# Optimization experiments

Measured on AMD Instinct MI355X. Metric: run time of the kernel, lower is better.

The kernel has to match this reference:

```python
import jax, jax.numpy as jnp
import numpy as np

N, E, IN_DIM, HID, OUT = 50000, 600000, 128, 256, 128

def setup_inputs() -> dict:
    key = jax.random.key(0)
    k1, k2, k3, k4, k5, k6, k7 = jax.random.split(key, 7)
    h = jax.random.normal(k1, (N, IN_DIM), dtype=jnp.float32)
    src = jax.random.randint(k2, (E,), 0, N)
    dst = jax.random.randint(k3, (E,), 0, N)
    s1 = 1.0 / np.sqrt(2 * IN_DIM)
    s2 = 1.0 / np.sqrt(HID)
    W1 = jax.random.uniform(k4, (2 * IN_DIM, HID), minval=-s1, maxval=s1, dtype=jnp.float32)
    b1 = jax.random.uniform(k5, (HID,), minval=-s1, maxval=s1, dtype=jnp.float32)
    W2 = jax.random.uniform(k6, (HID, OUT), minval=-s2, maxval=s2, dtype=jnp.float32)
    b2 = jax.random.uniform(k7, (OUT,), minval=-s2, maxval=s2, dtype=jnp.float32)
    return {"h": h, "src": src, "dst": dst, "W1": W1, "b1": b1, "W2": W2, "b2": b2}

def reference(h, src, dst, W1, b1, W2, b2):
    n = h.shape[0]
    # copy_u + mean: gather src features, segment-sum at dst, divide by in-degree
    msg_sum = jax.ops.segment_sum(h[src], dst, num_segments=n)          # [N, D]
    deg = jax.ops.segment_sum(jnp.ones((src.shape[0],), h.dtype), dst, num_segments=n)
    h_neigh = msg_sum / jnp.maximum(deg, 1.0)[:, None]                  # zero-deg nodes -> 0
    h_total = jnp.concatenate([h, h_neigh], axis=1)                     # [N, 2D]
    out = (h_total @ W1 + b1) @ W2 + b2                                 # 2-layer MLP (no inner activation)
    return jax.nn.relu(out)
```

## Files before the change

### kernel.cpp

```cpp
#include <hip/hip_runtime.h>

#define N_NODES 50000
#define E_EDGES 600000
#define IN_DIM  128
#define HID     256
#define OUT_DIM 128
#define CAP     64

#define NB_FILL 2344
#define NB_HCVT 6250
#define NB_WCVT 384

typedef __bf16 bf16x8 __attribute__((ext_vector_type(8)));
typedef float  f32x16 __attribute__((ext_vector_type(16)));

__device__ __forceinline__ unsigned short f2bf(float f) {
    union { float f; unsigned int i; } v; v.f = f;
    unsigned int b = v.i;
    b += 0x7fffu + ((b >> 16) & 1u);
    return (unsigned short)(b >> 16);
}
__device__ __forceinline__ float bf2f(unsigned short u) {
    union { unsigned int i; float f; } v; v.i = ((unsigned int)u) << 16; return v.f;
}

__global__ void __launch_bounds__(256)
sage_prep(const int* __restrict__ src, const int* __restrict__ dst,
          int* __restrict__ counts, int* __restrict__ bucket,
          const float* __restrict__ h, unsigned short* __restrict__ ht,
          const float* __restrict__ W1, const float* __restrict__ W2,
          unsigned short* __restrict__ w1sw, unsigned short* __restrict__ w2sw) {
    int b = blockIdx.x;
    if (b < NB_FILL) {
        int e = b * 256 + threadIdx.x;
        if (e < E_EDGES) {
            int d = dst[e];
            int slot = atomicAdd(counts + d, 1);
            if (slot < CAP) bucket[(size_t)d * CAP + slot] = src[e];
        }
    } else if (b < NB_FILL + NB_HCVT) {
        int idx = (b - NB_FILL) * 256 + threadIdx.x;
        if (idx < N_NODES * 32) {
            int n = idx >> 5, g = idx & 31;
            const float4 v = *(const float4*)(h + (size_t)n * IN_DIM + g * 4);
            ushort4 o;
            o.x = f2bf(v.x); o.y = f2bf(v.y); o.z = f2bf(v.z); o.w = f2bf(v.w);
            *(ushort4*)(ht + (size_t)n * 256 + g * 4) = o;
        }
    } else {
        int i = (b - NB_FILL - NB_HCVT) * 256 + threadIdx.x;
        if (i < 65536) {
            int j = i & 7, n = (i >> 3) & 255, g = (i >> 11) & 1, ks = (i >> 12) & 3, c = i >> 14;
            int k = c * 64 + ks * 16 + g * 8 + j;
            w1sw[i] = f2bf(W1[(size_t)k * HID + n]);
        } else {
            int i2 = i - 65536;
            int j = i2 & 7, n = (i2 >> 3) & 127, g = (i2 >> 10) & 1, ks = (i2 >> 11) & 7, c = (i2 >> 14) & 1;
            int k = c * 128 + ks * 16 + g * 8 + j;
            w2sw[i2] = f2bf(W2[(size_t)k * OUT_DIM + n]);
        }
    }
}

__global__ void __launch_bounds__(256)
sage_gather(const int* __restrict__ counts,
            const int* __restrict__ bucket,
            unsigned short* ht) {
    int node = blockIdx.x * 8 + (threadIdx.x >> 5);
    int l = threadIdx.x & 31;
    if (node >= N_NODES) return;

    int dg = counts[node];
    int entries = min(dg, CAP);
    const int* bk = bucket + (size_t)node * CAP;

    float a0 = 0.f, a1 = 0.f, a2 = 0.f, a3 = 0.f;
    int e = 0;
    for (; e + 4 <= entries; e += 4) {
        const int4 s = *(const int4*)(bk + e);
        const ushort4 v0 = *(const ushort4*)(ht + (size_t)s.x * 256 + l * 4);
        const ushort4 v1 = *(const ushort4*)(ht + (size_t)s.y * 256 + l * 4);
        const ushort4 v2 = *(const ushort4*)(ht + (size_t)s.z * 256 + l * 4);
        const ushort4 v3 = *(const ushort4*)(ht + (size_t)s.w * 256 + l * 4);
        a0 += bf2f(v0.x) + bf2f(v1.x) + bf2f(v2.x) + bf2f(v3.x);
        a1 += bf2f(v0.y) + bf2f(v1.y) + bf2f(v2.y) + bf2f(v3.y);
        a2 += bf2f(v0.z) + bf2f(v1.z) + bf2f(v2.z) + bf2f(v3.z);
        a3 += bf2f(v0.w) + bf2f(v1.w) + bf2f(v2.w) + bf2f(v3.w);
    }
    for (; e < entries; ++e) {
        const ushort4 v = *(const ushort4*)(ht + (size_t)bk[e] * 256 + l * 4);
        a0 += bf2f(v.x); a1 += bf2f(v.y); a2 += bf2f(v.z); a3 += bf2f(v.w);
    }
    float inv = 1.0f / (float)max(dg, 1);
    ushort4 o;
    o.x = f2bf(a0 * inv); o.y = f2bf(a1 * inv);
    o.z = f2bf(a2 * inv); o.w = f2bf(a3 * inv);
    *(ushort4*)(ht + (size_t)node * 256 + 128 + l * 4) = o;
}

__global__ void __launch_bounds__(256)
sage_mlp(const unsigned short* ht,
         const unsigned short* __restrict__ w1sw,
         const unsigned short* __restrict__ w2sw,
         const float* __restrict__ b1,
         const float* __restrict__ b2,
         float* out) {
    __shared__ unsigned short wbuf[16384];
    __shared__ unsigned short hid_s[64][264];

    const int t = threadIdx.x;
    const int nw = t >> 6;
    const int lane = t & 63;
    const int lr = lane & 31;
    const int lg = lane >> 5;
    const int base = blockIdx.x * 64;
    const int row0 = min(base + lr,      N_NODES - 1);
    const int row1 = min(base + 32 + lr, N_NODES - 1);

    f32x16 c1[2][2];
    #pragma unroll
    for (int e = 0; e < 16; ++e) {
        c1[0][0][e] = 0.f; c1[0][1][e] = 0.f; c1[1][0][e] = 0.f; c1[1][1][e] = 0.f;
    }

    #pragma unroll
    for (int c = 0; c < 4; ++c) {
        if (c) __syncthreads();
        {
            const bf16x8* gsrc = (const bf16x8*)(w1sw + c * 16384);
            #pragma unroll
            for (int i = 0; i < 8; ++i) {
                int off16 = i * 256 + t;
                *(bf16x8*)(wbuf + off16 * 8) = gsrc[off16];
            }
        }
        bf16x8 a0[4], a1[4];
        #pragma unroll
        for (int ks = 0; ks < 4; ++ks) {
            int koff = (c * 4 + ks) * 16 + lg * 8;
            a0[ks] = *(const bf16x8*)(ht + (size_t)row0 * 256 + koff);
            a1[ks] = *(const bf16x8*)(ht + (size_t)row1 * 256 + koff);
        }
        __syncthreads();
        #pragma unroll
        for (int ks = 0; ks < 4; ++ks) {
            #pragma unroll
            for (int nt = 0; nt < 2; ++nt) {
                int n = nw * 64 + nt * 32 + lr;
                bf16x8 b = *(const bf16x8*)(wbuf + (((ks * 2 + lg) * 256) + n) * 8);
                c1[0][nt] = __builtin_amdgcn_mfma_f32_32x32x16_bf16(a0[ks], b, c1[0][nt], 0, 0, 0);
                c1[1][nt] = __builtin_amdgcn_mfma_f32_32x32x16_bf16(a1[ks], b, c1[1][nt], 0, 0, 0);
            }
        }
    }

    #pragma unroll
    for (int nt = 0; nt < 2; ++nt) {
        int col = nw * 64 + nt * 32 + lr;
        float bias = b1[col];
        #pragma unroll
        for (int s = 0; s < 2; ++s) {
            #pragma unroll
            for (int reg = 0; reg < 16; ++reg) {
                int m = s * 32 + (reg & 3) + 8 * (reg >> 2) + 4 * lg;
                hid_s[m][col] = f2bf(c1[s][nt][reg] + bias);
            }
        }
    }
    __syncthreads();

    f32x16 c2[2];
    #pragma unroll
    for (int e = 0; e < 16; ++e) { c2[0][e] = 0.f; c2[1][e] = 0.f; }

    #pragma unroll
    for (int c = 0; c < 2; ++c) {
        if (c) __syncthreads();
        {
            const bf16x8* gsrc = (const bf16x8*)(w2sw + c * 16384);
            #pragma unroll
            for (int i = 0; i < 8; ++i) {
                int off16 = i * 256 + t;
                *(bf16x8*)(wbuf + off16 * 8) = gsrc[off16];
            }
        }
        __syncthreads();
        #pragma unroll
        for (int ks = 0; ks < 8; ++ks) {
            bf16x8 b = *(const bf16x8*)(wbuf + ((ks * 2 + lg) * 128 + nw * 32 + lr) * 8);
            int koff = c * 128 + ks * 16 + lg * 8;
            bf16x8 ah0 = *(const bf16x8*)(&hid_s[lr][koff]);
            bf16x8 ah1 = *(const bf16x8*)(&hid_s[32 + lr][koff]);
            c2[0] = __builtin_amdgcn_mfma_f32_32x32x16_bf16(ah0, b, c2[0], 0, 0, 0);
            c2[1] = __builtin_amdgcn_mfma_f32_32x32x16_bf16(ah1, b, c2[1], 0, 0, 0);
        }
    }

    {
        int col = nw * 32 + lr;
        float bias = b2[col];
        #pragma unroll
        for (int s = 0; s < 2; ++s) {
            #pragma unroll
            for (int reg = 0; reg < 16; ++reg) {
                int m = s * 32 + (reg & 3) + 8 * (reg >> 2) + 4 * lg;
                int n = base + m;
                if (n < N_NODES)
                    out[(size_t)n * OUT_DIM + col] = fmaxf(c2[s][reg] + bias, 0.0f);
            }
        }
    }
}

extern "C" void kernel_launch(void* const* d_in, const int* in_sizes, int n_in,
                              void* d_out, int out_size, void* d_ws, size_t ws_size,
                              hipStream_t stream) {
    const float* h   = (const float*)d_in[0];
    const int*   src = (const int*)d_in[1];
    const int*   dst = (const int*)d_in[2];
    const float* W1  = (const float*)d_in[3];
    const float* b1  = (const float*)d_in[4];
    const float* W2  = (const float*)d_in[5];
    const float* b2  = (const float*)d_in[6];
    float* out = (float*)d_out;

    unsigned short* ht = (unsigned short*)d_out;

    int* counts = (int*)d_ws;
    int* bucket = counts + N_NODES;
    unsigned short* w1sw = (unsigned short*)(bucket + (size_t)N_NODES * CAP);
    unsigned short* w2sw = w1sw + 65536;

    hipMemsetAsync(counts, 0, N_NODES * sizeof(int), stream);

    sage_prep<<<NB_FILL + NB_HCVT + NB_WCVT, 256, 0, stream>>>(
        src, dst, counts, bucket, h, ht, W1, W2, w1sw, w2sw);

    sage_gather<<<(N_NODES + 7) / 8, 256, 0, stream>>>(counts, bucket, ht);

    sage_mlp<<<(N_NODES + 63) / 64, 256, 0, stream>>>(ht, w1sw, w2sw, b1, b2, out);
}
```

Before: 182.3 us.

## Fuse neighbor-mean gather into MLP kernel and store buckets in output buffer

```diff
diff --git a/kernel.cpp b/kernel.cpp
--- a/kernel.cpp
+++ b/kernel.cpp
@@ -10,9 +10,12 @@
 #define NB_FILL 2344
 #define NB_HCVT 6250
 #define NB_WCVT 384
+#define NB_PREP (NB_FILL + NB_HCVT + NB_WCVT)
+#define NB_MLP  782
 
 typedef __bf16 bf16x8 __attribute__((ext_vector_type(8)));
 typedef float  f32x16 __attribute__((ext_vector_type(16)));
+typedef unsigned short ushort8 __attribute__((ext_vector_type(8)));
 
 __device__ __forceinline__ unsigned short f2bf(float f) {
     union { float f; unsigned int i; } v; v.f = f;
@@ -26,35 +29,46 @@
 
 __global__ void __launch_bounds__(256)
 sage_prep(const int* __restrict__ src, const int* __restrict__ dst,
-          int* __restrict__ counts, int* __restrict__ bucket,
+          int* __restrict__ counts, char* __restrict__ outb,
           const float* __restrict__ h, unsigned short* __restrict__ ht,
           const float* __restrict__ W1, const float* __restrict__ W2,
           unsigned short* __restrict__ w1sw, unsigned short* __restrict__ w2sw) {
-    int b = blockIdx.x;
-    if (b < NB_FILL) {
-        int e = b * 256 + threadIdx.x;
+    int i = blockIdx.x;
+    int q = i >> 2, r = i & 3;
+    int job, id;
+    if (r == 1) { job = 0; id = q; }
+    else {
+        int oid = 3 * q + (r == 0 ? 0 : r - 1);
+        if (oid < NB_HCVT)           { job = 1; id = oid; }
+        else if (oid < NB_HCVT + NB_WCVT) { job = 2; id = oid - NB_HCVT; }
+        else                         { job = 0; id = 2245 + (oid - (NB_HCVT + NB_WCVT)); }
+    }
+
+    if (job == 0) {
+        int e = id * 256 + threadIdx.x;
         if (e < E_EDGES) {
             int d = dst[e];
             int slot = atomicAdd(counts + d, 1);
-            if (slot < CAP) bucket[(size_t)d * CAP + slot] = src[e];
-        }
-    } else if (b < NB_FILL + NB_HCVT) {
-        int idx = (b - NB_FILL) * 256 + threadIdx.x;
+            if (slot < CAP)
+                *((int*)(outb + (size_t)d * 512 + 256) + slot) = src[e];
+        }
+    } else if (job == 1) {
+        int idx = id * 256 + threadIdx.x;
         if (idx < N_NODES * 32) {
             int n = idx >> 5, g = idx & 31;
             const float4 v = *(const float4*)(h + (size_t)n * IN_DIM + g * 4);
             ushort4 o;
             o.x = f2bf(v.x); o.y = f2bf(v.y); o.z = f2bf(v.z); o.w = f2bf(v.w);
-            *(ushort4*)(ht + (size_t)n * 256 + g * 4) = o;
+            *(ushort4*)(ht + (size_t)n * 128 + g * 4) = o;
         }
     } else {
-        int i = (b - NB_FILL - NB_HCVT) * 256 + threadIdx.x;
-        if (i < 65536) {
-            int j = i & 7, n = (i >> 3) & 255, g = (i >> 11) & 1, ks = (i >> 12) & 3, c = i >> 14;
+        int i1 = id * 256 + threadIdx.x;
+        if (i1 < 65536) {
+            int j = i1 & 7, n = (i1 >> 3) & 255, g = (i1 >> 11) & 1, ks = (i1 >> 12) & 3, c = i1 >> 14;
             int k = c * 64 + ks * 16 + g * 8 + j;
-            w1sw[i] = f2bf(W1[(size_t)k * HID + n]);
+            w1sw[i1] = f2bf(W1[(size_t)k * HID + n]);
         } else {
-            int i2 = i - 65536;
+            int i2 = i1 - 65536;
             int j = i2 & 7, n = (i2 >> 3) & 127, g = (i2 >> 10) & 1, ks = (i2 >> 11) & 7, c = (i2 >> 14) & 1;
             int k = c * 128 + ks * 16 + g * 8 + j;
             w2sw[i2] = f2bf(W2[(size_t)k * OUT_DIM + n]);
@@ -63,48 +77,13 @@
 }
 
 __global__ void __launch_bounds__(256)
-sage_gather(const int* __restrict__ counts,
-            const int* __restrict__ bucket,
-            unsigned short* ht) {
-    int node = blockIdx.x * 8 + (threadIdx.x >> 5);
-    int l = threadIdx.x & 31;
-    if (node >= N_NODES) return;
-
-    int dg = counts[node];
-    int entries = min(dg, CAP);
-    const int* bk = bucket + (size_t)node * CAP;
-
-    float a0 = 0.f, a1 = 0.f, a2 = 0.f, a3 = 0.f;
-    int e = 0;
-    for (; e + 4 <= entries; e += 4) {
-        const int4 s = *(const int4*)(bk + e);
-        const ushort4 v0 = *(const ushort4*)(ht + (size_t)s.x * 256 + l * 4);
-        const ushort4 v1 = *(const ushort4*)(ht + (size_t)s.y * 256 + l * 4);
-        const ushort4 v2 = *(const ushort4*)(ht + (size_t)s.z * 256 + l * 4);
-        const ushort4 v3 = *(const ushort4*)(ht + (size_t)s.w * 256 + l * 4);
-        a0 += bf2f(v0.x) + bf2f(v1.x) + bf2f(v2.x) + bf2f(v3.x);
-        a1 += bf2f(v0.y) + bf2f(v1.y) + bf2f(v2.y) + bf2f(v3.y);
-        a2 += bf2f(v0.z) + bf2f(v1.z) + bf2f(v2.z) + bf2f(v3.z);
-        a3 += bf2f(v0.w) + bf2f(v1.w) + bf2f(v2.w) + bf2f(v3.w);
-    }
-    for (; e < entries; ++e) {
-        const ushort4 v = *(const ushort4*)(ht + (size_t)bk[e] * 256 + l * 4);
-        a0 += bf2f(v.x); a1 += bf2f(v.y); a2 += bf2f(v.z); a3 += bf2f(v.w);
-    }
-    float inv = 1.0f / (float)max(dg, 1);
-    ushort4 o;
-    o.x = f2bf(a0 * inv); o.y = f2bf(a1 * inv);
-    o.z = f2bf(a2 * inv); o.w = f2bf(a3 * inv);
-    *(ushort4*)(ht + (size_t)node * 256 + 128 + l * 4) = o;
-}
-
-__global__ void __launch_bounds__(256)
-sage_mlp(const unsigned short* ht,
-         const unsigned short* __restrict__ w1sw,
-         const unsigned short* __restrict__ w2sw,
-         const float* __restrict__ b1,
-         const float* __restrict__ b2,
-         float* out) {
+sage_fused(const int* __restrict__ counts,
+           const unsigned short* __restrict__ ht,
+           const unsigned short* __restrict__ w1sw,
+           const unsigned short* __restrict__ w2sw,
+           const float* __restrict__ b1,
+           const float* __restrict__ b2,
+           float* out) {
     __shared__ unsigned short wbuf[16384];
     __shared__ unsigned short hid_s[64][264];
 
@@ -117,29 +96,96 @@
     const int row0 = min(base + lr,      N_NODES - 1);
     const int row1 = min(base + 32 + lr, N_NODES - 1);
 
+    {
+        const bf16x8* gsrc = (const bf16x8*)(w1sw);
+        #pragma unroll
+        for (int i2 = 0; i2 < 8; ++i2) {
+            int off16 = i2 * 256 + t;
+            *(bf16x8*)(wbuf + off16 * 8) = gsrc[off16];
+        }
+    }
+
+    {
+        int node = base + (t >> 2);
+        int l4 = t & 3;
+        if (node < N_NODES) {
+            int dg = counts[node];
+            int entries = min(dg, CAP);
+            const int* bk = (const int*)((const char*)out + (size_t)node * 512 + 256);
+            float acc[32];
+            #pragma unroll
+            for (int j = 0; j < 32; ++j) acc[j] = 0.f;
+            int e = 0;
+            for (; e + 4 <= entries; e += 4) {
+                const int4 sx = *(const int4*)(bk + e);
+                const ushort8* p0 = (const ushort8*)(ht + (size_t)sx.x * 128 + l4 * 32);
+                const ushort8* p1 = (const ushort8*)(ht + (size_t)sx.y * 128 + l4 * 32);
+                const ushort8* p2 = (const ushort8*)(ht + (size_t)sx.z * 128 + l4 * 32);
+                const ushort8* p3 = (const ushort8*)(ht + (size_t)sx.w * 128 + l4 * 32);
+                ushort8 v00 = p0[0], v01 = p0[1], v02 = p0[2], v03 = p0[3];
+                ushort8 v10 = p1[0], v11 = p1[1], v12 = p1[2], v13 = p1[3];
+                ushort8 v20 = p2[0], v21 = p2[1], v22 = p2[2], v23 = p2[3];
+                ushort8 v30 = p3[0], v31 = p3[1], v32 = p3[2], v33 = p3[3];
+                #pragma unroll
+                for (int j = 0; j < 8; ++j) {
+                    acc[j]      += bf2f(v00[j]) + bf2f(v10[j]) + bf2f(v20[j]) + bf2f(v30[j]);
+                    acc[8 + j]  += bf2f(v01[j]) + bf2f(v11[j]) + bf2f(v21[j]) + bf2f(v31[j]);
+                    acc[16 + j] += bf2f(v02[j]) + bf2f(v12[j]) + bf2f(v22[j]) + bf2f(v32[j]);
+                    acc[24 + j] += bf2f(v03[j]) + bf2f(v13[j]) + bf2f(v23[j]) + bf2f(v33[j]);
+                }
+            }
+            for (; e < entries; ++e) {
+                const ushort8* p = (const ushort8*)(ht + (size_t)bk[e] * 128 + l4 * 32);
+                ushort8 w0 = p[0], w1v = p[1], w2v = p[2], w3 = p[3];
+                #pragma unroll
+                for (int j = 0; j < 8; ++j) {
+                    acc[j]      += bf2f(w0[j]);
+                    acc[8 + j]  += bf2f(w1v[j]);
+                    acc[16 + j] += bf2f(w2v[j]);
+                    acc[24 + j] += bf2f(w3[j]);
+                }
+            }
+            float inv = 1.0f / (float)max(dg, 1);
+            int m = t >> 2;
+            #pragma unroll
+            for (int qq = 0; qq < 4; ++qq) {
+                ushort8 o;
+                #pragma unroll
+                for (int j = 0; j < 8; ++j) o[j] = f2bf(acc[qq * 8 + j] * inv);
+                *(ushort8*)(&hid_s[m][l4 * 32 + qq * 8]) = o;
+            }
+        }
+    }
+
     f32x16 c1[2][2];
     #pragma unroll
-    for (int e = 0; e < 16; ++e) {
-        c1[0][0][e] = 0.f; c1[0][1][e] = 0.f; c1[1][0][e] = 0.f; c1[1][1][e] = 0.f;
+    for (int e2 = 0; e2 < 16; ++e2) {
+        c1[0][0][e2] = 0.f; c1[0][1][e2] = 0.f; c1[1][0][e2] = 0.f; c1[1][1][e2] = 0.f;
     }
 
     #pragma unroll
     for (int c = 0; c < 4; ++c) {
-        if (c) __syncthreads();
-        {
+        if (c) {
+            __syncthreads();
             const bf16x8* gsrc = (const bf16x8*)(w1sw + c * 16384);
             #pragma unroll
-            for (int i = 0; i < 8; ++i) {
-                int off16 = i * 256 + t;
+            for (int i2 = 0; i2 < 8; ++i2) {
+                int off16 = i2 * 256 + t;
                 *(bf16x8*)(wbuf + off16 * 8) = gsrc[off16];
             }
         }
         bf16x8 a0[4], a1[4];
         #pragma unroll
         for (int ks = 0; ks < 4; ++ks) {
-            int koff = (c * 4 + ks) * 16 + lg * 8;
-            a0[ks] = *(const bf16x8*)(ht + (size_t)row0 * 256 + koff);
-            a1[ks] = *(const bf16x8*)(ht + (size_t)row1 * 256 + koff);
+            if (c < 2) {
+                int koff = (c * 4 + ks) * 16 + lg * 8;
+                a0[ks] = *(const bf16x8*)(ht + (size_t)row0 * 128 + koff);
+                a1[ks] = *(const bf16x8*)(ht + (size_t)row1 * 128 + koff);
+            } else {
+                int koff = (c - 2) * 64 + ks * 16 + lg * 8;
+                a0[ks] = *(const bf16x8*)(&hid_s[lr][koff]);
+                a1[ks] = *(const bf16x8*)(&hid_s[32 + lr][koff]);
+            }
         }
         __syncthreads();
         #pragma unroll
@@ -171,7 +217,7 @@
 
     f32x16 c2[2];
     #pragma unroll
-    for (int e = 0; e < 16; ++e) { c2[0][e] = 0.f; c2[1][e] = 0.f; }
+    for (int e2 = 0; e2 < 16; ++e2) { c2[0][e2] = 0.f; c2[1][e2] = 0.f; }
 
     #pragma unroll
     for (int c = 0; c < 2; ++c) {
@@ -179,8 +225,8 @@
         {
             const bf16x8* gsrc = (const bf16x8*)(w2sw + c * 16384);
             #pragma unroll
-            for (int i = 0; i < 8; ++i) {
-                int off16 = i * 256 + t;
+            for (int i2 = 0; i2 < 8; ++i2) {
+                int off16 = i2 * 256 + t;
                 *(bf16x8*)(wbuf + off16 * 8) = gsrc[off16];
             }
         }
@@ -224,19 +270,15 @@
     const float* b2  = (const float*)d_in[6];
     float* out = (float*)d_out;
 
-    unsigned short* ht = (unsigned short*)d_out;
-
     int* counts = (int*)d_ws;
-    int* bucket = counts + N_NODES;
-    unsigned short* w1sw = (unsigned short*)(bucket + (size_t)N_NODES * CAP);
+    unsigned short* w1sw = (unsigned short*)(counts + N_NODES);
     unsigned short* w2sw = w1sw + 65536;
+    unsigned short* ht   = w2sw + 32768;
 
     hipMemsetAsync(counts, 0, N_NODES * sizeof(int), stream);
 
-    sage_prep<<<NB_FILL + NB_HCVT + NB_WCVT, 256, 0, stream>>>(
-        src, dst, counts, bucket, h, ht, W1, W2, w1sw, w2sw);
-
-    sage_gather<<<(N_NODES + 7) / 8, 256, 0, stream>>>(counts, bucket, ht);
-
-    sage_mlp<<<(N_NODES + 63) / 64, 256, 0, stream>>>(ht, w1sw, w2sw, b1, b2, out);
-}
+    sage_prep<<<NB_PREP, 256, 0, stream>>>(
+        src, dst, counts, (char*)d_out, h, ht, W1, W2, w1sw, w2sw);
+
+    sage_fused<<<NB_MLP, 256, 0, stream>>>(counts, ht, w1sw, w2sw, b1, b2, out);
+}
```

New measurement: 183.9 us. No clear change (+0.9%).
